# Kernel optimization log

Measured on AMD Instinct MI355X. Metric: run time of the kernel, lower is better.

## Reference

```python
import jax, jax.numpy as jnp
import numpy as np
import math

H = 8  # num_heads
SCALE = 1.0 / math.sqrt(512.0)  # original divides by sqrt(dim_V), not sqrt(head_dim)


def setup_inputs() -> dict:
    key = jax.random.key(0)
    ks = jax.random.split(key, 16)
    B, N, D = 32, 512, 512
    s = 1.0 / math.sqrt(D)
    return {
        "Q": jax.random.normal(ks[0], (B, N, D), jnp.float32),
        "K": jax.random.normal(ks[1], (B, N, D), jnp.float32),
        "Wq": jax.random.normal(ks[2], (D, D), jnp.float32) * s,
        "bq": jnp.zeros((D,), jnp.float32),
        "Wk": jax.random.normal(ks[3], (D, D), jnp.float32) * s,
        "bk": jnp.zeros((D,), jnp.float32),
        "Wv": jax.random.normal(ks[4], (D, D), jnp.float32) * s,
        "bv": jnp.zeros((D,), jnp.float32),
        "Wo": jax.random.normal(ks[5], (D, D), jnp.float32) * s,
        "bo": jnp.zeros((D,), jnp.float32),
        "W1": jax.random.normal(ks[6], (D, D), jnp.float32) * s,
        "b1": jnp.zeros((D,), jnp.float32),
        "W2": jax.random.normal(ks[7], (D, D), jnp.float32) * s,
        "b2": jnp.zeros((D,), jnp.float32),
    }


def reference(Q, K, Wq, bq, Wk, bk, Wv, bv, Wo, bo, W1, b1, W2, b2):
    B, Nq, D = Q.shape
    dh = D // H
    # projections (torch Linear: x @ W.T + b)
    q = (Q @ Wq.T + bq).reshape(B, Nq, H, dh)
    k = (K @ Wk.T + bk).reshape(B, K.shape[1], H, dh)
    v = (K @ Wv.T + bv).reshape(B, K.shape[1], H, dh)
    # scores: [B, H, Nq, Nk], scaled by 1/sqrt(dim_V)
    scores = jnp.einsum("bqhd,bkhd->bhqk", q, k) * SCALE
    # NOTE: original softmax is over dim=1 of [H*B, Nq, Nk] == the QUERY axis
    A = jax.nn.softmax(scores, axis=2)
    attn = jnp.einsum("bhqk,bkhd->bqhd", A, v).reshape(B, Nq, D)
    out = Q + (attn @ Wo.T + bo)  # dropout p=0.0
    ffn = jax.nn.relu(out @ W1.T + b1) @ W2.T + b2
    return out + ffn
```

## Files before the change

### kernel.cpp

```cpp
#include <hip/hip_runtime.h>
#include <stdint.h>

#define SCALE_ 0.044194173824159216f
#define QSC_ (0.044194173824159216f * 1.4426950408889634f)

typedef __attribute__((ext_vector_type(8))) short bf16x8;
typedef __attribute__((ext_vector_type(4))) float f32x4;
typedef __attribute__((ext_vector_type(16))) float f32x16;
typedef __attribute__((ext_vector_type(2))) unsigned int uint2v;

__device__ __forceinline__ ushort f2b(float f) {
  union { float f; uint32_t u; } v; v.f = f;
  return (ushort)((v.u + 0x7fffu + ((v.u >> 16) & 1u)) >> 16);
}
__device__ __forceinline__ uint32_t cvtpk(float lo, float hi) {
  uint32_t r; asm("v_cvt_pk_bf16_f32 %0, %1, %2" : "=v"(r) : "v"(lo), "v"(hi)); return r;
}
__device__ __forceinline__ float ex2(float x) {
  float r; asm("v_exp_f32 %0, %1" : "=v"(r) : "v"(x)); return r;
}
__device__ __forceinline__ void gld16(void* lds, const void* g) {
  __builtin_amdgcn_global_load_lds(
      (const __attribute__((address_space(1))) uint32_t*)g,
      (__attribute__((address_space(3))) uint32_t*)lds, 16, 0, 0);
}

__global__ __launch_bounds__(256)
void k_cvt(const float* __restrict__ Q, const float* __restrict__ K,
           const float* __restrict__ w0, const float* __restrict__ w1,
           const float* __restrict__ w2, const float* __restrict__ w3,
           const float* __restrict__ w4, const float* __restrict__ w5,
           ushort* __restrict__ Qb, ushort* __restrict__ Kb, ushort* __restrict__ Wb)
{
  const long long NQ = 8388608LL, NW = 262144LL;
  long long i = ((long long)blockIdx.x * 256 + threadIdx.x) * 4;
  const float* src; ushort* dst; long long off;
  if (i < NQ)        { src = Q; dst = Qb; off = i; }
  else if (i < 2*NQ) { src = K; dst = Kb; off = i - NQ; }
  else {
    long long j = i - 2*NQ; int seg = (int)(j / NW); off = j - (long long)seg * NW;
    switch (seg) { case 0: src = w0; break; case 1: src = w1; break; case 2: src = w2; break;
                   case 3: src = w3; break; case 4: src = w4; break; default: src = w5; }
    dst = Wb + (size_t)seg * NW;
  }
  float4 v = *(const float4*)(src + off);
  ushort4 o = make_ushort4(f2b(v.x), f2b(v.y), f2b(v.z), f2b(v.w));
  *(ushort4*)(dst + off) = o;
}

template<int EPI>
__device__ __forceinline__ void gemm_body(const ushort* __restrict__ A, const ushort* __restrict__ Bw,
                                          const float* __restrict__ bias, const float* __restrict__ extra,
                                          float* __restrict__ outf, ushort* __restrict__ outb,
                                          char* lds, int m0, int n0, float os)
{
  const int t = threadIdx.x;
  const int w = t >> 6, lane = t & 63;
  const int wm = w >> 1, wn = w & 1;
  const int rA = lane & 15, g = lane >> 4;

  const ushort* srcA[4]; int ldsA[4];
#pragma unroll
  for (int j = 0; j < 4; j++) {
    int L = (t + j*512) * 16;
    int U = L ^ (((L >> 7) & 7) << 4);
    srcA[j] = A + (size_t)(m0 + (U >> 7))*512 + ((U & 127) >> 1);
    ldsA[j] = L;
  }
  const ushort* srcB[2]; int ldsB[2];
#pragma unroll
  for (int j = 0; j < 2; j++) {
    int L = (t + j*512) * 16;
    int U = L ^ (((L >> 7) & 7) << 4);
    srcB[j] = Bw + (size_t)(n0 + (U >> 7))*512 + ((U & 127) >> 1);
    ldsB[j] = 32768 + L;
  }

#define STAGE_A(ti) do { char* bb_ = lds + ((ti) % 3) * 49152; \
    _Pragma("unroll") \
    for (int j = 0; j < 4; j++) gld16(bb_ + ldsA[j], srcA[j] + (ti)*64); } while (0)
#define STAGE_B(ti) do { char* bb_ = lds + ((ti) % 3) * 49152; \
    _Pragma("unroll") \
    for (int j = 0; j < 2; j++) gld16(bb_ + ldsB[j], srcB[j] + (ti)*64); } while (0)

  STAGE_A(0); STAGE_B(0);
  STAGE_A(1); STAGE_B(1);

  f32x4 acc[4][4] = {};
  for (int i = 0; i < 8; i++) {
    if (i < 7) asm volatile("s_waitcnt vmcnt(6)" ::: "memory");
    else       asm volatile("s_waitcnt vmcnt(0)" ::: "memory");
    __builtin_amdgcn_s_barrier();
    __builtin_amdgcn_sched_barrier(0);
    const char* bufc = lds + (i % 3) * 49152;

    bf16x8 afA[4], bfA[4];
#pragma unroll
    for (int m = 0; m < 4; m++) {
      int row = wm*64 + m*16 + rA;
      afA[m] = *(const bf16x8*)(bufc + ((row*128 + g*16) ^ ((row & 7) << 4)));
    }
#pragma unroll
    for (int n = 0; n < 4; n++) {
      int row = wn*64 + n*16 + rA;
      bfA[n] = *(const bf16x8*)(bufc + 32768 + ((row*128 + g*16) ^ ((row & 7) << 4)));
    }
    if (i < 6) STAGE_A(i + 2);
    __builtin_amdgcn_s_barrier();
    __builtin_amdgcn_sched_barrier(0);

    bf16x8 afB[4], bfB[4];
#pragma unroll
    for (int m = 0; m < 4; m++) {
      int row = wm*64 + m*16 + rA;
      afB[m] = *(const bf16x8*)(bufc + ((row*128 + 64 + g*16) ^ ((row & 7) << 4)));
    }
#pragma unroll
    for (int n = 0; n < 4; n++) {
      int row = wn*64 + n*16 + rA;
      bfB[n] = *(const bf16x8*)(bufc + 32768 + ((row*128 + 64 + g*16) ^ ((row & 7) << 4)));
    }
    if (i < 6) STAGE_B(i + 2);
    __builtin_amdgcn_s_setprio(1);
#pragma unroll
    for (int m = 0; m < 4; m++)
#pragma unroll
      for (int n = 0; n < 4; n++)
        acc[m][n] = __builtin_amdgcn_mfma_f32_16x16x32_bf16(afA[m], bfA[n], acc[m][n], 0, 0, 0);
    __builtin_amdgcn_s_setprio(0);
    __builtin_amdgcn_s_barrier();
    __builtin_amdgcn_sched_barrier(0);

    __builtin_amdgcn_s_setprio(1);
#pragma unroll
    for (int m = 0; m < 4; m++)
#pragma unroll
      for (int n = 0; n < 4; n++)
        acc[m][n] = __builtin_amdgcn_mfma_f32_16x16x32_bf16(afB[m], bfB[n], acc[m][n], 0, 0, 0);
    __builtin_amdgcn_s_setprio(0);
  }
#undef STAGE_A
#undef STAGE_B

#pragma unroll
  for (int m = 0; m < 4; m++)
#pragma unroll
    for (int n = 0; n < 4; n++) {
      int col = n0 + wn*64 + n*16 + rA;
      float bb = bias[col];
      if (EPI == 4) {
        int b = m0 >> 9, k0 = m0 & 511;
        int hh = col >> 6, dl = col & 63;
        int kg = k0 + wm*64 + m*16 + g*4;
        float v0 = acc[m][n][0] + bb, v1 = acc[m][n][1] + bb;
        float v2 = acc[m][n][2] + bb, v3 = acc[m][n][3] + bb;
        uint2 pk;
        pk.x = (uint32_t)f2b(v0) | ((uint32_t)f2b(v1) << 16);
        pk.y = (uint32_t)f2b(v2) | ((uint32_t)f2b(v3) << 16);
        *(uint2*)(outb + ((size_t)((b*8 + hh)*64 + dl)*512 + kg)) = pk;
      } else {
#pragma unroll
        for (int r = 0; r < 4; r++) {
          int row = m0 + wm*64 + m*16 + g*4 + r;
          size_t idx = (size_t)row*512 + col;
          float v = acc[m][n][r] + bb;
          if (EPI == 0)      outb[idx] = f2b(v * os);
          else if (EPI == 1) { float o = extra[idx] + v; outf[idx] = o; outb[idx] = f2b(o); }
          else if (EPI == 2) outb[idx] = f2b(v > 0.f ? v : 0.f);
          else               outf[idx] += v;
        }
      }
    }
}

template<int EPI>
__global__ __launch_bounds__(512, 2)
void k_gemm(const ushort* __restrict__ A, const ushort* __restrict__ Bw,
            const float* __restrict__ bias, const float* __restrict__ extra,
            float* __restrict__ outf, ushort* __restrict__ outb)
{
  __shared__ __align__(16) char lds[3*49152];
  gemm_body<EPI>(A, Bw, bias, extra, outf, outb, lds, blockIdx.x*256, blockIdx.y*128, 1.0f);
}

__global__ __launch_bounds__(512, 2)
void k_gemm_qkv(const ushort* __restrict__ Qb, const ushort* __restrict__ Kb,
                const ushort* __restrict__ Wb, const float* __restrict__ bq,
                const float* __restrict__ bk, const float* __restrict__ bvv,
                ushort* __restrict__ qkout, ushort* __restrict__ vpT)
{
  __shared__ __align__(16) char lds[3*49152];
  int z = blockIdx.z;
  if (z == 2) {
    gemm_body<4>(Kb, Wb + 2*(size_t)262144, bvv, nullptr, nullptr,
                 vpT, lds, blockIdx.x*256, blockIdx.y*128, 1.0f);
  } else {
    const ushort* A = (z == 0) ? Qb : Kb;
    const float* bias = (z == 0) ? bq : bk;
    float os = (z == 0) ? QSC_ : 1.0f;
    gemm_body<0>(A, Wb + (size_t)z*262144, bias, nullptr, nullptr,
                 qkout + (size_t)z*8388608, lds, blockIdx.x*256, blockIdx.y*128, os);
  }
}

__global__ __launch_bounds__(512, 2)
void k_att2(const ushort* __restrict__ qp, const ushort* __restrict__ kp,
            const ushort* __restrict__ vpT, float* __restrict__ zinv,
            ushort* __restrict__ attn)
{
  __shared__ __align__(16) char kt[65536];
  __shared__ __align__(16) char vt[65536];
  __shared__ __align__(16) char qpr[32768];
  int bh = blockIdx.x;
  int b = bh >> 3, h = bh & 7;
  int t = threadIdx.x, w = t >> 6, lane = t & 63;
  int rA = lane & 15, g = lane >> 4;
  const ushort* kbase = kp + (size_t)(b*512)*512 + h*64;
  const ushort* qbase = qp + (size_t)(b*512)*512 + h*64;
  const ushort* vbase = vpT + (size_t)bh*64*512;

#pragma unroll
  for (int i = 0; i < 8; i++) {
    int c = i*512 + t; int row = c >> 3, sl = c & 7;
    gld16(kt + c*16, kbase + (size_t)row*512 + ((sl ^ (row & 7))*8));
  }
#define STAGE_Q(buf, qb) do { \
    _Pragma("unroll") \
    for (int i = 0; i < 2; i++) { \
      int c = i*512 + t; int row = c >> 3, sl = c & 7; \
      gld16(qpr + (buf)*16384 + c*16, \
            qbase + (size_t)((qb)*128 + row)*512 + ((sl ^ (row & 7))*8)); } } while (0)
  STAGE_Q(0, 0);
  STAGE_Q(1, 1);
#pragma unroll
  for (int i = 0; i < 8; i++) {
    int c = i*512 + t; int d = c >> 6, sl = c & 63;
    gld16(vt + c*16, vbase + (size_t)d*512 + ((sl ^ (d & 7))*8));
  }

  asm volatile("s_waitcnt vmcnt(10)" ::: "memory");
  __builtin_amdgcn_s_barrier();
  __builtin_amdgcn_sched_barrier(0);
  bf16x8 kf[4][2];
#pragma unroll
  for (int n = 0; n < 4; n++)
#pragma unroll
    for (int ks = 0; ks < 2; ks++) {
      int k = w*64 + n*16 + rA;
      kf[n][ks] = *(const bf16x8*)(kt + k*128 + (((ks*4 + g) ^ (k & 7))*16));
    }
  float Zacc[4] = {0.f, 0.f, 0.f, 0.f};
  for (int qb = 0; qb < 4; qb++) {
    if (qb == 1)      { asm volatile("s_waitcnt vmcnt(10)" ::: "memory"); }
    else if (qb == 2) { asm volatile("s_waitcnt vmcnt(2)" ::: "memory"); }
    else if (qb == 3) { asm volatile("s_waitcnt vmcnt(0)" ::: "memory"); }
    if (qb) { __builtin_amdgcn_s_barrier(); __builtin_amdgcn_sched_barrier(0); }
    const char* qtb = qpr + (qb & 1)*16384;
    f32x4 acc[8][4] = {};
#pragma unroll
    for (int ks = 0; ks < 2; ks++) {
      bf16x8 af[8];
#pragma unroll
      for (int m = 0; m < 8; m++) {
        int q = m*16 + rA;
        af[m] = *(const bf16x8*)(qtb + q*128 + (((ks*4 + g) ^ (q & 7))*16));
      }
      __builtin_amdgcn_s_setprio(1);
#pragma unroll
      for (int m = 0; m < 8; m++)
#pragma unroll
        for (int n = 0; n < 4; n++)
          acc[m][n] = __builtin_amdgcn_mfma_f32_16x16x32_bf16(af[m], kf[n][ks], acc[m][n], 0, 0, 0);
      __builtin_amdgcn_s_setprio(0);
    }
    if (qb < 3) __builtin_amdgcn_s_barrier();
    if (qb < 2) STAGE_Q(qb & 1, qb + 2);
#pragma unroll
    for (int m = 0; m < 8; m++)
#pragma unroll
      for (int n = 0; n < 4; n++) {
        float s = 0.f;
#pragma unroll
        for (int r = 0; r < 4; r++) s += ex2(acc[m][n][r]);
        Zacc[n] += s;
      }
  }
#undef STAGE_Q
#pragma unroll
  for (int n = 0; n < 4; n++) {
    float v = Zacc[n];
    v += __shfl_xor(v, 16);
    v += __shfl_xor(v, 32);
    if (lane < 16) ((float*)qpr)[w*64 + n*16 + lane] = 1.0f / v;
  }
  __syncthreads();

  const int l31 = lane & 31, hi5 = lane >> 5;
  bf16x8 qf2[2][4];
#pragma unroll
  for (int qb = 0; qb < 2; qb++)
#pragma unroll
    for (int ksd = 0; ksd < 4; ksd++)
      qf2[qb][ksd] = *(const bf16x8*)(qbase + (size_t)(w*64 + qb*32 + l31)*512 + ksd*16 + hi5*8);
  const float* zl = (const float*)qpr;
  f32x16 oacc[2][2] = {};
  for (int kc = 0; kc < 16; kc++) {
    bf16x8 kf2[4];
#pragma unroll
    for (int ksd = 0; ksd < 4; ksd++) {
      int k = kc*32 + l31;
      kf2[ksd] = *(const bf16x8*)(kt + k*128 + (((ksd*2 + hi5) ^ (k & 7))*16));
    }
    bf16x8 vf2[2][2];
#pragma unroll
    for (int db = 0; db < 2; db++)
#pragma unroll
      for (int ks = 0; ks < 2; ks++) {
        int d = db*32 + l31;
        vf2[db][ks] = *(const bf16x8*)(vt + d*1024 + (((kc*4 + ks*2 + hi5) ^ (d & 7))*16));
      }
    f32x4 zv[4];
#pragma unroll
    for (int j = 0; j < 4; j++)
      zv[j] = *(const f32x4*)(zl + kc*32 + j*8 + hi5*4);
#pragma unroll
    for (int qb = 0; qb < 2; qb++) {
      f32x16 s = {};
      __builtin_amdgcn_s_setprio(1);
#pragma unroll
      for (int ksd = 0; ksd < 4; ksd++)
        s = __builtin_amdgcn_mfma_f32_32x32x16_bf16(kf2[ksd], qf2[qb][ksd], s, 0, 0, 0);
      __builtin_amdgcn_s_setprio(0);
      float e[16];
#pragma unroll
      for (int r = 0; r < 16; r++) e[r] = ex2(s[r]) * zv[r >> 2][r & 3];
      uint32_t x0 = cvtpk(e[0], e[1]),   y0 = cvtpk(e[4], e[5]);
      uint32_t x1 = cvtpk(e[2], e[3]),   y1 = cvtpk(e[6], e[7]);
      uint32_t x2 = cvtpk(e[8], e[9]),   y2 = cvtpk(e[12], e[13]);
      uint32_t x3 = cvtpk(e[10], e[11]), y3 = cvtpk(e[14], e[15]);
      uint2v r0 = __builtin_amdgcn_permlane32_swap(x0, y0, false, false);
      uint2v r1 = __builtin_amdgcn_permlane32_swap(x1, y1, false, false);
      uint2v r2 = __builtin_amdgcn_permlane32_swap(x2, y2, false, false);
      uint2v r3 = __builtin_amdgcn_permlane32_swap(x3, y3, false, false);
      union { uint32_t u[4]; bf16x8 v; } p0, p1;
      p0.u[0] = r0[0]; p0.u[1] = r1[0]; p0.u[2] = r0[1]; p0.u[3] = r1[1];
      p1.u[0] = r2[0]; p1.u[1] = r3[0]; p1.u[2] = r2[1]; p1.u[3] = r3[1];
      __builtin_amdgcn_s_setprio(1);
#pragma unroll
      for (int db = 0; db < 2; db++) {
        oacc[qb][db] = __builtin_amdgcn_mfma_f32_32x32x16_bf16(p0.v, vf2[db][0], oacc[qb][db], 0, 0, 0);
        oacc[qb][db] = __builtin_amdgcn_mfma_f32_32x32x16_bf16(p1.v, vf2[db][1], oacc[qb][db], 0, 0, 0);
      }
      __builtin_amdgcn_s_setprio(0);
    }
  }
#pragma unroll
  for (int qb = 0; qb < 2; qb++)
#pragma unroll
    for (int db = 0; db < 2; db++)
#pragma unroll
      for (int r = 0; r < 16; r++) {
        int q = w*64 + qb*32 + (r & 3) + 8*(r >> 2) + 4*hi5;
        int d = db*32 + l31;
        attn[(size_t)(b*512 + q)*512 + h*64 + d] = f2b(oacc[qb][db][r]);
      }
}

extern "C" void kernel_launch(void* const* d_in, const int* in_sizes, int n_in,
                              void* d_out, int out_size, void* d_ws, size_t ws_size,
                              hipStream_t stream) {
  const float* Q  = (const float*)d_in[0];
  const float* K  = (const float*)d_in[1];
  const float* Wq = (const float*)d_in[2];
  const float* bq = (const float*)d_in[3];
  const float* Wk = (const float*)d_in[4];
  const float* bk = (const float*)d_in[5];
  const float* Wv = (const float*)d_in[6];
  const float* bv = (const float*)d_in[7];
  const float* Wo = (const float*)d_in[8];
  const float* bo = (const float*)d_in[9];
  const float* W1 = (const float*)d_in[10];
  const float* b1 = (const float*)d_in[11];
  const float* W2 = (const float*)d_in[12];
  const float* b2 = (const float*)d_in[13];
  float* out = (float*)d_out;

  const size_t SZ = (size_t)16384 * 512;
  ushort* Qb   = (ushort*)d_ws;
  ushort* Kb   = Qb + SZ;
  ushort* qp   = Kb + SZ;
  ushort* kp   = qp + SZ;
  ushort* vpT  = kp + SZ;
  ushort* Wb   = vpT + SZ;
  float*  zinv = (float*)(Wb + 6 * (size_t)262144);
  ushort* attn = Qb;
  ushort* outb = Kb;
  ushort* h1   = vpT;

  k_cvt<<<dim3(17920), dim3(256), 0, stream>>>(Q, K, Wq, Wk, Wv, Wo, W1, W2, Qb, Kb, Wb);
  k_gemm_qkv<<<dim3(64, 4, 3), dim3(512), 0, stream>>>(Qb, Kb, Wb, bq, bk, bv, qp, vpT);
  k_att2<<<dim3(256), dim3(512), 0, stream>>>(qp, kp, vpT, zinv, attn);
  k_gemm<1><<<dim3(64, 4), dim3(512), 0, stream>>>(attn, Wb + 3*(size_t)262144, bo, Q, out, outb);
  k_gemm<2><<<dim3(64, 4), dim3(512), 0, stream>>>(outb, Wb + 4*(size_t)262144, b1, nullptr, nullptr, h1);
  k_gemm<3><<<dim3(64, 4), dim3(512), 0, stream>>>(h1, Wb + 5*(size_t)262144, b2, nullptr, out, nullptr);
}
```

Before: 148.3 us.

## Fuse fp32-to-bf16 conversion of Q/K into QKV projection GEMM loads

The separate conversion pass over Q and K is removed. The QKV GEMM now loads fp32 activations into registers, packs them to bf16 with v_cvt_pk_bf16_f32, and writes them to swizzled LDS, software-pipelined two tiles ahead. Weights keep a small dedicated conversion kernel. The generic GEMM main loop is also restructured to load both K-halves of fragments and issue all staging before one barrier, cutting barriers per iteration. The cost is extra register pressure and VALU/LDS-store work inside the QKV GEMM, and K is re-read as fp32 by two GEMM z-slices.

```diff
diff --git a/kernel.cpp b/kernel.cpp
--- a/kernel.cpp
+++ b/kernel.cpp
@@ -26,33 +26,28 @@
 }
 
 __global__ __launch_bounds__(256)
-void k_cvt(const float* __restrict__ Q, const float* __restrict__ K,
-           const float* __restrict__ w0, const float* __restrict__ w1,
-           const float* __restrict__ w2, const float* __restrict__ w3,
-           const float* __restrict__ w4, const float* __restrict__ w5,
-           ushort* __restrict__ Qb, ushort* __restrict__ Kb, ushort* __restrict__ Wb)
+void k_cvtw(const float* __restrict__ w0, const float* __restrict__ w1,
+            const float* __restrict__ w2, const float* __restrict__ w3,
+            const float* __restrict__ w4, const float* __restrict__ w5,
+            ushort* __restrict__ Wb)
 {
-  const long long NQ = 8388608LL, NW = 262144LL;
-  long long i = ((long long)blockIdx.x * 256 + threadIdx.x) * 4;
-  const float* src; ushort* dst; long long off;
-  if (i < NQ)        { src = Q; dst = Qb; off = i; }
-  else if (i < 2*NQ) { src = K; dst = Kb; off = i - NQ; }
-  else {
-    long long j = i - 2*NQ; int seg = (int)(j / NW); off = j - (long long)seg * NW;
-    switch (seg) { case 0: src = w0; break; case 1: src = w1; break; case 2: src = w2; break;
-                   case 3: src = w3; break; case 4: src = w4; break; default: src = w5; }
-    dst = Wb + (size_t)seg * NW;
-  }
+  const int NW = 262144;
+  int i = (blockIdx.x * 256 + threadIdx.x) * 4;
+  int seg = i >> 18;
+  int off = i & (NW - 1);
+  const float* src;
+  switch (seg) { case 0: src = w0; break; case 1: src = w1; break; case 2: src = w2; break;
+                 case 3: src = w3; break; case 4: src = w4; break; default: src = w5; }
   float4 v = *(const float4*)(src + off);
   ushort4 o = make_ushort4(f2b(v.x), f2b(v.y), f2b(v.z), f2b(v.w));
-  *(ushort4*)(dst + off) = o;
+  *(ushort4*)(Wb + (size_t)seg * NW + off) = o;
 }
 
 template<int EPI>
 __device__ __forceinline__ void gemm_body(const ushort* __restrict__ A, const ushort* __restrict__ Bw,
                                           const float* __restrict__ bias, const float* __restrict__ extra,
                                           float* __restrict__ outf, ushort* __restrict__ outb,
-                                          char* lds, int m0, int n0, float os)
+                                          char* lds, int m0, int n0)
 {
   const int t = threadIdx.x;
   const int w = t >> 6, lane = t & 63;
@@ -94,44 +89,27 @@
     __builtin_amdgcn_sched_barrier(0);
     const char* bufc = lds + (i % 3) * 49152;
 
-    bf16x8 afA[4], bfA[4];
+    bf16x8 afA[4], bfA[4], afB[4], bfB[4];
 #pragma unroll
     for (int m = 0; m < 4; m++) {
       int row = wm*64 + m*16 + rA;
       afA[m] = *(const bf16x8*)(bufc + ((row*128 + g*16) ^ ((row & 7) << 4)));
+      afB[m] = *(const bf16x8*)(bufc + ((row*128 + 64 + g*16) ^ ((row & 7) << 4)));
     }
 #pragma unroll
     for (int n = 0; n < 4; n++) {
       int row = wn*64 + n*16 + rA;
       bfA[n] = *(const bf16x8*)(bufc + 32768 + ((row*128 + g*16) ^ ((row & 7) << 4)));
-    }
-    if (i < 6) STAGE_A(i + 2);
-    __builtin_amdgcn_s_barrier();
+      bfB[n] = *(const bf16x8*)(bufc + 32768 + ((row*128 + 64 + g*16) ^ ((row & 7) << 4)));
+    }
+    if (i < 6) { STAGE_A(i + 2); STAGE_B(i + 2); }
     __builtin_amdgcn_sched_barrier(0);
-
-    bf16x8 afB[4], bfB[4];
-#pragma unroll
-    for (int m = 0; m < 4; m++) {
-      int row = wm*64 + m*16 + rA;
-      afB[m] = *(const bf16x8*)(bufc + ((row*128 + 64 + g*16) ^ ((row & 7) << 4)));
-    }
-#pragma unroll
-    for (int n = 0; n < 4; n++) {
-      int row = wn*64 + n*16 + rA;
-      bfB[n] = *(const bf16x8*)(bufc + 32768 + ((row*128 + 64 + g*16) ^ ((row & 7) << 4)));
-    }
-    if (i < 6) STAGE_B(i + 2);
     __builtin_amdgcn_s_setprio(1);
 #pragma unroll
     for (int m = 0; m < 4; m++)
 #pragma unroll
       for (int n = 0; n < 4; n++)
         acc[m][n] = __builtin_amdgcn_mfma_f32_16x16x32_bf16(afA[m], bfA[n], acc[m][n], 0, 0, 0);
-    __builtin_amdgcn_s_setprio(0);
-    __builtin_amdgcn_s_barrier();
-    __builtin_amdgcn_sched_barrier(0);
-
-    __builtin_amdgcn_s_setprio(1);
 #pragma unroll
     for (int m = 0; m < 4; m++)
 #pragma unroll
@@ -141,6 +119,144 @@
   }
 #undef STAGE_A
 #undef STAGE_B
+
+#pragma unroll
+  for (int m = 0; m < 4; m++)
+#pragma unroll
+    for (int n = 0; n < 4; n++) {
+      int col = n0 + wn*64 + n*16 + rA;
+      float bb = bias[col];
+#pragma unroll
+      for (int r = 0; r < 4; r++) {
+        int row = m0 + wm*64 + m*16 + g*4 + r;
+        size_t idx = (size_t)row*512 + col;
+        float v = acc[m][n][r] + bb;
+        if (EPI == 1)      { float o = extra[idx] + v; outf[idx] = o; outb[idx] = f2b(o); }
+        else if (EPI == 2) outb[idx] = f2b(v > 0.f ? v : 0.f);
+        else               outf[idx] += v;
+      }
+    }
+}
+
+template<int EPI>
+__global__ __launch_bounds__(512, 2)
+void k_gemm(const ushort* __restrict__ A, const ushort* __restrict__ Bw,
+            const float* __restrict__ bias, const float* __restrict__ extra,
+            float* __restrict__ outf, ushort* __restrict__ outb)
+{
+  __shared__ __align__(16) char lds[3*49152];
+  gemm_body<EPI>(A, Bw, bias, extra, outf, outb, lds, blockIdx.x*256, blockIdx.y*128);
+}
+
+template<int EPI>
+__device__ __forceinline__ void gemm_f32a_body(const float* __restrict__ A32, const ushort* __restrict__ Bw,
+                                               const float* __restrict__ bias,
+                                               float* __restrict__ outf, ushort* __restrict__ outb,
+                                               char* lds, int m0, int n0, float os)
+{
+  const int t = threadIdx.x;
+  const int w = t >> 6, lane = t & 63;
+  const int wm = w >> 1, wn = w & 1;
+  const int rA = lane & 15, g = lane >> 4;
+
+  const float* srcA[4]; int ldsA[4];
+#pragma unroll
+  for (int j = 0; j < 4; j++) {
+    int L = (t + j*512) * 16;
+    int U = L ^ (((L >> 7) & 7) << 4);
+    srcA[j] = A32 + (size_t)(m0 + (U >> 7))*512 + ((U & 127) >> 1);
+    ldsA[j] = L;
+  }
+  const ushort* srcB[2]; int ldsB[2];
+#pragma unroll
+  for (int j = 0; j < 2; j++) {
+    int L = (t + j*512) * 16;
+    int U = L ^ (((L >> 7) & 7) << 4);
+    srcB[j] = Bw + (size_t)(n0 + (U >> 7))*512 + ((U & 127) >> 1);
+    ldsB[j] = 32768 + L;
+  }
+
+#define QLA(ti, R) do { \
+    _Pragma("unroll") \
+    for (int j = 0; j < 4; j++) { \
+      R[2*j]   = *(const float4*)(srcA[j] + (ti)*64); \
+      R[2*j+1] = *(const float4*)(srcA[j] + (ti)*64 + 4); } } while (0)
+#define QWA(ti, R) do { char* bb_ = lds + ((ti) % 3) * 49152; \
+    _Pragma("unroll") \
+    for (int j = 0; j < 4; j++) { \
+      uint4 qq; \
+      qq.x = cvtpk(R[2*j].x,   R[2*j].y); \
+      qq.y = cvtpk(R[2*j].z,   R[2*j].w); \
+      qq.z = cvtpk(R[2*j+1].x, R[2*j+1].y); \
+      qq.w = cvtpk(R[2*j+1].z, R[2*j+1].w); \
+      *(uint4*)(bb_ + ldsA[j]) = qq; } } while (0)
+#define QSB(ti) do { char* bb_ = lds + ((ti) % 3) * 49152; \
+    _Pragma("unroll") \
+    for (int j = 0; j < 2; j++) gld16(bb_ + ldsB[j], srcB[j] + (ti)*64); } while (0)
+
+  float4 a0[8], a1[8];
+  QLA(0, a0);
+  __builtin_amdgcn_sched_barrier(0);
+  QLA(1, a1);
+  __builtin_amdgcn_sched_barrier(0);
+  QSB(0); QSB(1);
+  __builtin_amdgcn_sched_barrier(0);
+  asm volatile("s_waitcnt vmcnt(12)" ::: "memory");
+  QWA(0, a0);
+
+  f32x4 acc[4][4] = {};
+
+#define QITER(i, RI, RW) do { \
+    if ((i) == 0)      asm volatile("s_waitcnt vmcnt(2) lgkmcnt(0)" ::: "memory"); \
+    else if ((i) == 7) asm volatile("s_waitcnt vmcnt(0) lgkmcnt(0)" ::: "memory"); \
+    else               asm volatile("s_waitcnt vmcnt(10) lgkmcnt(0)" ::: "memory"); \
+    __builtin_amdgcn_s_barrier(); \
+    __builtin_amdgcn_sched_barrier(0); \
+    const char* bufc = lds + ((i) % 3) * 49152; \
+    bf16x8 afA[4], bfA[4], afB[4], bfB[4]; \
+    _Pragma("unroll") \
+    for (int m = 0; m < 4; m++) { \
+      int row = wm*64 + m*16 + rA; \
+      afA[m] = *(const bf16x8*)(bufc + ((row*128 + g*16) ^ ((row & 7) << 4))); \
+      afB[m] = *(const bf16x8*)(bufc + ((row*128 + 64 + g*16) ^ ((row & 7) << 4))); \
+    } \
+    _Pragma("unroll") \
+    for (int n = 0; n < 4; n++) { \
+      int row = wn*64 + n*16 + rA; \
+      bfA[n] = *(const bf16x8*)(bufc + 32768 + ((row*128 + g*16) ^ ((row & 7) << 4))); \
+      bfB[n] = *(const bf16x8*)(bufc + 32768 + ((row*128 + 64 + g*16) ^ ((row & 7) << 4))); \
+    } \
+    if ((i) < 6) QLA((i) + 2, RI); \
+    __builtin_amdgcn_sched_barrier(0); \
+    if ((i) < 7) QWA((i) + 1, RW); \
+    if ((i) < 6) QSB((i) + 2); \
+    __builtin_amdgcn_sched_barrier(0); \
+    __builtin_amdgcn_s_setprio(1); \
+    _Pragma("unroll") \
+    for (int m = 0; m < 4; m++) \
+      _Pragma("unroll") \
+      for (int n = 0; n < 4; n++) \
+        acc[m][n] = __builtin_amdgcn_mfma_f32_16x16x32_bf16(afA[m], bfA[n], acc[m][n], 0, 0, 0); \
+    _Pragma("unroll") \
+    for (int m = 0; m < 4; m++) \
+      _Pragma("unroll") \
+      for (int n = 0; n < 4; n++) \
+        acc[m][n] = __builtin_amdgcn_mfma_f32_16x16x32_bf16(afB[m], bfB[n], acc[m][n], 0, 0, 0); \
+    __builtin_amdgcn_s_setprio(0); \
+  } while (0)
+
+  QITER(0, a0, a1);
+  QITER(1, a1, a0);
+  QITER(2, a0, a1);
+  QITER(3, a1, a0);
+  QITER(4, a0, a1);
+  QITER(5, a1, a0);
+  QITER(6, a0, a1);
+  QITER(7, a1, a0);
+#undef QITER
+#undef QLA
+#undef QWA
+#undef QSB
 
 #pragma unroll
   for (int m = 0; m < 4; m++)
@@ -163,43 +279,29 @@
         for (int r = 0; r < 4; r++) {
           int row = m0 + wm*64 + m*16 + g*4 + r;
           size_t idx = (size_t)row*512 + col;
-          float v = acc[m][n][r] + bb;
-          if (EPI == 0)      outb[idx] = f2b(v * os);
-          else if (EPI == 1) { float o = extra[idx] + v; outf[idx] = o; outb[idx] = f2b(o); }
-          else if (EPI == 2) outb[idx] = f2b(v > 0.f ? v : 0.f);
-          else               outf[idx] += v;
+          outb[idx] = f2b((acc[m][n][r] + bb) * os);
         }
       }
     }
 }
 
-template<int EPI>
 __global__ __launch_bounds__(512, 2)
-void k_gemm(const ushort* __restrict__ A, const ushort* __restrict__ Bw,
-            const float* __restrict__ bias, const float* __restrict__ extra,
-            float* __restrict__ outf, ushort* __restrict__ outb)
-{
-  __shared__ __align__(16) char lds[3*49152];
-  gemm_body<EPI>(A, Bw, bias, extra, outf, outb, lds, blockIdx.x*256, blockIdx.y*128, 1.0f);
-}
-
-__global__ __launch_bounds__(512, 2)
-void k_gemm_qkv(const ushort* __restrict__ Qb, const ushort* __restrict__ Kb,
-                const ushort* __restrict__ Wb, const float* __restrict__ bq,
-                const float* __restrict__ bk, const float* __restrict__ bvv,
-                ushort* __restrict__ qkout, ushort* __restrict__ vpT)
+void k_gemm_qkvf(const float* __restrict__ Qf, const float* __restrict__ Kf,
+                 const ushort* __restrict__ Wb, const float* __restrict__ bq,
+                 const float* __restrict__ bk, const float* __restrict__ bvv,
+                 ushort* __restrict__ qkout, ushort* __restrict__ vpT)
 {
   __shared__ __align__(16) char lds[3*49152];
   int z = blockIdx.z;
   if (z == 2) {
-    gemm_body<4>(Kb, Wb + 2*(size_t)262144, bvv, nullptr, nullptr,
-                 vpT, lds, blockIdx.x*256, blockIdx.y*128, 1.0f);
+    gemm_f32a_body<4>(Kf, Wb + 2*(size_t)262144, bvv, nullptr, vpT,
+                      lds, blockIdx.x*256, blockIdx.y*128, 1.0f);
+  } else if (z == 1) {
+    gemm_f32a_body<0>(Kf, Wb + (size_t)262144, bk, nullptr, qkout + (size_t)8388608,
+                      lds, blockIdx.x*256, blockIdx.y*128, 1.0f);
   } else {
-    const ushort* A = (z == 0) ? Qb : Kb;
-    const float* bias = (z == 0) ? bq : bk;
-    float os = (z == 0) ? QSC_ : 1.0f;
-    gemm_body<0>(A, Wb + (size_t)z*262144, bias, nullptr, nullptr,
-                 qkout + (size_t)z*8388608, lds, blockIdx.x*256, blockIdx.y*128, os);
+    gemm_f32a_body<0>(Qf, Wb, bq, nullptr, qkout,
+                      lds, blockIdx.x*256, blockIdx.y*128, QSC_);
   }
 }
 
@@ -386,19 +488,17 @@
   float* out = (float*)d_out;
 
   const size_t SZ = (size_t)16384 * 512;
-  ushort* Qb   = (ushort*)d_ws;
-  ushort* Kb   = Qb + SZ;
-  ushort* qp   = Kb + SZ;
+  ushort* attn = (ushort*)d_ws;
+  ushort* outb = attn + SZ;
+  ushort* qp   = outb + SZ;
   ushort* kp   = qp + SZ;
   ushort* vpT  = kp + SZ;
   ushort* Wb   = vpT + SZ;
   float*  zinv = (float*)(Wb + 6 * (size_t)262144);
-  ushort* attn = Qb;
-  ushort* outb = Kb;
   ushort* h1   = vpT;
 
-  k_cvt<<<dim3(17920), dim3(256), 0, stream>>>(Q, K, Wq, Wk, Wv, Wo, W1, W2, Qb, Kb, Wb);
-  k_gemm_qkv<<<dim3(64, 4, 3), dim3(512), 0, stream>>>(Qb, Kb, Wb, bq, bk, bv, qp, vpT);
+  k_cvtw<<<dim3(1536), dim3(256), 0, stream>>>(Wq, Wk, Wv, Wo, W1, W2, Wb);
+  k_gemm_qkvf<<<dim3(64, 4, 3), dim3(512), 0, stream>>>(Q, K, Wb, bq, bk, bv, qp, vpT);
   k_att2<<<dim3(256), dim3(512), 0, stream>>>(qp, kp, vpT, zinv, attn);
   k_gemm<1><<<dim3(64, 4), dim3(512), 0, stream>>>(attn, Wb + 3*(size_t)262144, bo, Q, out, outb);
   k_gemm<2><<<dim3(64, 4), dim3(512), 0, stream>>>(outb, Wb + 4*(size_t)262144, b1, nullptr, nullptr, h1);
```

Result: no change. 146.5 us (-1.2%).

## Fuse fp32-to-bf16 conversion of Q/K into projection GEMMs and share K tiles for K/V

Applied to the files above, without the earlier changes.

The separate pass that converted the full Q and K activations to bf16 is removed. The projection GEMMs now stream fp32 A tiles into LDS and convert them to bf16 in registers before the MFMAs. The K and V projections are fused into one kernel that reuses each loaded K tile against both weight matrices. The shared GEMM loop is also simplified to one barrier and one staging step per k-step. This is meant to remove a large read-and-write round trip through memory, at the cost of double the A-tile LDS traffic, lower occupancy (launch bounds of 1) and extra register pressure from the dual accumulators.

```diff
diff --git a/kernel.cpp b/kernel.cpp
--- a/kernel.cpp
+++ b/kernel.cpp
@@ -26,33 +26,28 @@
 }
 
 __global__ __launch_bounds__(256)
-void k_cvt(const float* __restrict__ Q, const float* __restrict__ K,
-           const float* __restrict__ w0, const float* __restrict__ w1,
-           const float* __restrict__ w2, const float* __restrict__ w3,
-           const float* __restrict__ w4, const float* __restrict__ w5,
-           ushort* __restrict__ Qb, ushort* __restrict__ Kb, ushort* __restrict__ Wb)
-{
-  const long long NQ = 8388608LL, NW = 262144LL;
-  long long i = ((long long)blockIdx.x * 256 + threadIdx.x) * 4;
-  const float* src; ushort* dst; long long off;
-  if (i < NQ)        { src = Q; dst = Qb; off = i; }
-  else if (i < 2*NQ) { src = K; dst = Kb; off = i - NQ; }
-  else {
-    long long j = i - 2*NQ; int seg = (int)(j / NW); off = j - (long long)seg * NW;
-    switch (seg) { case 0: src = w0; break; case 1: src = w1; break; case 2: src = w2; break;
-                   case 3: src = w3; break; case 4: src = w4; break; default: src = w5; }
-    dst = Wb + (size_t)seg * NW;
-  }
+void k_cvtw(const float* __restrict__ w0, const float* __restrict__ w1,
+            const float* __restrict__ w2, const float* __restrict__ w3,
+            const float* __restrict__ w4, const float* __restrict__ w5,
+            ushort* __restrict__ Wb)
+{
+  const int NW = 262144;
+  int i = (blockIdx.x * 256 + threadIdx.x) * 4;
+  int seg = i >> 18;
+  int off = i & (NW - 1);
+  const float* src;
+  switch (seg) { case 0: src = w0; break; case 1: src = w1; break; case 2: src = w2; break;
+                 case 3: src = w3; break; case 4: src = w4; break; default: src = w5; }
   float4 v = *(const float4*)(src + off);
   ushort4 o = make_ushort4(f2b(v.x), f2b(v.y), f2b(v.z), f2b(v.w));
-  *(ushort4*)(dst + off) = o;
+  *(ushort4*)(Wb + (size_t)seg * NW + off) = o;
 }
 
 template<int EPI>
 __device__ __forceinline__ void gemm_body(const ushort* __restrict__ A, const ushort* __restrict__ Bw,
                                           const float* __restrict__ bias, const float* __restrict__ extra,
                                           float* __restrict__ outf, ushort* __restrict__ outb,
-                                          char* lds, int m0, int n0, float os)
+                                          char* lds, int m0, int n0)
 {
   const int t = threadIdx.x;
   const int w = t >> 6, lane = t & 63;
@@ -76,15 +71,13 @@
     ldsB[j] = 32768 + L;
   }
 
-#define STAGE_A(ti) do { char* bb_ = lds + ((ti) % 3) * 49152; \
+#define STAGE_T(ti) do { char* bb_ = lds + ((ti) % 3) * 49152; \
     _Pragma("unroll") \
-    for (int j = 0; j < 4; j++) gld16(bb_ + ldsA[j], srcA[j] + (ti)*64); } while (0)
-#define STAGE_B(ti) do { char* bb_ = lds + ((ti) % 3) * 49152; \
+    for (int j = 0; j < 4; j++) gld16(bb_ + ldsA[j], srcA[j] + (ti)*64); \
     _Pragma("unroll") \
     for (int j = 0; j < 2; j++) gld16(bb_ + ldsB[j], srcB[j] + (ti)*64); } while (0)
 
-  STAGE_A(0); STAGE_B(0);
-  STAGE_A(1); STAGE_B(1);
+  STAGE_T(0); STAGE_T(1);
 
   f32x4 acc[4][4] = {};
   for (int i = 0; i < 8; i++) {
@@ -94,44 +87,27 @@
     __builtin_amdgcn_sched_barrier(0);
     const char* bufc = lds + (i % 3) * 49152;
 
-    bf16x8 afA[4], bfA[4];
+    bf16x8 afA[4], bfA[4], afB[4], bfB[4];
 #pragma unroll
     for (int m = 0; m < 4; m++) {
       int row = wm*64 + m*16 + rA;
       afA[m] = *(const bf16x8*)(bufc + ((row*128 + g*16) ^ ((row & 7) << 4)));
+      afB[m] = *(const bf16x8*)(bufc + ((row*128 + 64 + g*16) ^ ((row & 7) << 4)));
     }
 #pragma unroll
     for (int n = 0; n < 4; n++) {
       int row = wn*64 + n*16 + rA;
       bfA[n] = *(const bf16x8*)(bufc + 32768 + ((row*128 + g*16) ^ ((row & 7) << 4)));
-    }
-    if (i < 6) STAGE_A(i + 2);
-    __builtin_amdgcn_s_barrier();
+      bfB[n] = *(const bf16x8*)(bufc + 32768 + ((row*128 + 64 + g*16) ^ ((row & 7) << 4)));
+    }
+    if (i < 6) STAGE_T(i + 2);
     __builtin_amdgcn_sched_barrier(0);
-
-    bf16x8 afB[4], bfB[4];
-#pragma unroll
-    for (int m = 0; m < 4; m++) {
-      int row = wm*64 + m*16 + rA;
-      afB[m] = *(const bf16x8*)(bufc + ((row*128 + 64 + g*16) ^ ((row & 7) << 4)));
-    }
-#pragma unroll
-    for (int n = 0; n < 4; n++) {
-      int row = wn*64 + n*16 + rA;
-      bfB[n] = *(const bf16x8*)(bufc + 32768 + ((row*128 + 64 + g*16) ^ ((row & 7) << 4)));
-    }
-    if (i < 6) STAGE_B(i + 2);
     __builtin_amdgcn_s_setprio(1);
 #pragma unroll
     for (int m = 0; m < 4; m++)
 #pragma unroll
       for (int n = 0; n < 4; n++)
         acc[m][n] = __builtin_amdgcn_mfma_f32_16x16x32_bf16(afA[m], bfA[n], acc[m][n], 0, 0, 0);
-    __builtin_amdgcn_s_setprio(0);
-    __builtin_amdgcn_s_barrier();
-    __builtin_amdgcn_sched_barrier(0);
-
-    __builtin_amdgcn_s_setprio(1);
 #pragma unroll
     for (int m = 0; m < 4; m++)
 #pragma unroll
@@ -139,8 +115,7 @@
         acc[m][n] = __builtin_amdgcn_mfma_f32_16x16x32_bf16(afB[m], bfB[n], acc[m][n], 0, 0, 0);
     __builtin_amdgcn_s_setprio(0);
   }
-#undef STAGE_A
-#undef STAGE_B
+#undef STAGE_T
 
 #pragma unroll
   for (int m = 0; m < 4; m++)
@@ -148,27 +123,14 @@
     for (int n = 0; n < 4; n++) {
       int col = n0 + wn*64 + n*16 + rA;
       float bb = bias[col];
-      if (EPI == 4) {
-        int b = m0 >> 9, k0 = m0 & 511;
-        int hh = col >> 6, dl = col & 63;
-        int kg = k0 + wm*64 + m*16 + g*4;
-        float v0 = acc[m][n][0] + bb, v1 = acc[m][n][1] + bb;
-        float v2 = acc[m][n][2] + bb, v3 = acc[m][n][3] + bb;
-        uint2 pk;
-        pk.x = (uint32_t)f2b(v0) | ((uint32_t)f2b(v1) << 16);
-        pk.y = (uint32_t)f2b(v2) | ((uint32_t)f2b(v3) << 16);
-        *(uint2*)(outb + ((size_t)((b*8 + hh)*64 + dl)*512 + kg)) = pk;
-      } else {
-#pragma unroll
-        for (int r = 0; r < 4; r++) {
-          int row = m0 + wm*64 + m*16 + g*4 + r;
-          size_t idx = (size_t)row*512 + col;
-          float v = acc[m][n][r] + bb;
-          if (EPI == 0)      outb[idx] = f2b(v * os);
-          else if (EPI == 1) { float o = extra[idx] + v; outf[idx] = o; outb[idx] = f2b(o); }
-          else if (EPI == 2) outb[idx] = f2b(v > 0.f ? v : 0.f);
-          else               outf[idx] += v;
-        }
+#pragma unroll
+      for (int r = 0; r < 4; r++) {
+        int row = m0 + wm*64 + m*16 + g*4 + r;
+        size_t idx = (size_t)row*512 + col;
+        float v = acc[m][n][r] + bb;
+        if (EPI == 1)      { float o = extra[idx] + v; outf[idx] = o; outb[idx] = f2b(o); }
+        else if (EPI == 2) outb[idx] = f2b(v > 0.f ? v : 0.f);
+        else               outf[idx] += v;
       }
     }
 }
@@ -180,27 +142,149 @@
             float* __restrict__ outf, ushort* __restrict__ outb)
 {
   __shared__ __align__(16) char lds[3*49152];
-  gemm_body<EPI>(A, Bw, bias, extra, outf, outb, lds, blockIdx.x*256, blockIdx.y*128, 1.0f);
-}
-
-__global__ __launch_bounds__(512, 2)
-void k_gemm_qkv(const ushort* __restrict__ Qb, const ushort* __restrict__ Kb,
-                const ushort* __restrict__ Wb, const float* __restrict__ bq,
-                const float* __restrict__ bk, const float* __restrict__ bvv,
-                ushort* __restrict__ qkout, ushort* __restrict__ vpT)
+  gemm_body<EPI>(A, Bw, bias, extra, outf, outb, lds, blockIdx.x*256, blockIdx.y*128);
+}
+
+template<int DUAL>
+__device__ __forceinline__ void proj_body(const float* __restrict__ A32, const ushort* __restrict__ B0w,
+                                          const ushort* __restrict__ B1w,
+                                          const float* __restrict__ bias0, const float* __restrict__ bias1,
+                                          ushort* __restrict__ out0, ushort* __restrict__ vpT,
+                                          char* lds, int m0, int n0, float os)
+{
+  const int t = threadIdx.x;
+  const int w = t >> 6, lane = t & 63;
+  const int wm = w >> 1, wn = w & 1;
+  const int rA = lane & 15, g = lane >> 4;
+  const int BUF = DUAL ? 49152 : 40960;
+  const int L = DUAL ? 6 : 5;
+
+  const float* srcA[4]; int ldsA[4];
+#pragma unroll
+  for (int j = 0; j < 4; j++) {
+    int Lb = (t + j*512) * 16;
+    int U = Lb ^ (((Lb >> 7) & 7) << 4);
+    srcA[j] = A32 + (size_t)(m0 + (U >> 7))*512 + ((U & 127) >> 2);
+    ldsA[j] = Lb;
+  }
+  const ushort* srcB0; const ushort* srcB1; int ldsB;
+  {
+    int Lb = t * 16;
+    int U = Lb ^ (((Lb >> 6) & 3) << 4);
+    int row = U >> 6, col = (U & 63) >> 1;
+    srcB0 = B0w + (size_t)(n0 + row)*512 + col;
+    srcB1 = DUAL ? (B1w + (size_t)(n0 + row)*512 + col) : srcB0;
+    ldsB = 32768 + Lb;
+  }
+
+#define PSTAGE(ti) do { char* bb_ = lds + ((ti) % 3) * BUF; \
+    _Pragma("unroll") \
+    for (int j = 0; j < 4; j++) gld16(bb_ + ldsA[j], srcA[j] + (ti)*32); \
+    gld16(bb_ + ldsB, srcB0 + (ti)*32); \
+    if (DUAL) gld16(bb_ + 8192 + ldsB, srcB1 + (ti)*32); } while (0)
+
+  PSTAGE(0); PSTAGE(1);
+
+  f32x4 acc0[4][4] = {};
+  f32x4 acc1[4][4] = {};
+  for (int i = 0; i < 16; i++) {
+    if (i < 15) { if (DUAL) asm volatile("s_waitcnt vmcnt(6)" ::: "memory");
+                  else      asm volatile("s_waitcnt vmcnt(5)" ::: "memory"); }
+    else          asm volatile("s_waitcnt vmcnt(0)" ::: "memory");
+    __builtin_amdgcn_s_barrier();
+    __builtin_amdgcn_sched_barrier(0);
+    const char* bufc = lds + (i % 3) * BUF;
+
+    bf16x8 af[4];
+#pragma unroll
+    for (int m = 0; m < 4; m++) {
+      int row = wm*64 + m*16 + rA;
+      int o0 = (row*128 + g*32) ^ ((row & 7) << 4);
+      f32x4 lo = *(const f32x4*)(bufc + o0);
+      f32x4 hi = *(const f32x4*)(bufc + (o0 ^ 16));
+      union { uint32_t u[4]; bf16x8 v; } af_;
+      af_.u[0] = cvtpk(lo[0], lo[1]); af_.u[1] = cvtpk(lo[2], lo[3]);
+      af_.u[2] = cvtpk(hi[0], hi[1]); af_.u[3] = cvtpk(hi[2], hi[3]);
+      af[m] = af_.v;
+    }
+    bf16x8 bf0[4];
+#pragma unroll
+    for (int n = 0; n < 4; n++) {
+      int row = wn*64 + n*16 + rA;
+      bf0[n] = *(const bf16x8*)(bufc + 32768 + ((row*64 + g*16) ^ ((row & 3) << 4)));
+    }
+    if (i < 14) PSTAGE(i + 2);
+    __builtin_amdgcn_sched_barrier(0);
+    __builtin_amdgcn_s_setprio(1);
+#pragma unroll
+    for (int m = 0; m < 4; m++)
+#pragma unroll
+      for (int n = 0; n < 4; n++)
+        acc0[m][n] = __builtin_amdgcn_mfma_f32_16x16x32_bf16(af[m], bf0[n], acc0[m][n], 0, 0, 0);
+    __builtin_amdgcn_s_setprio(0);
+    if (DUAL) {
+      bf16x8 bf1[4];
+#pragma unroll
+      for (int n = 0; n < 4; n++) {
+        int row = wn*64 + n*16 + rA;
+        bf1[n] = *(const bf16x8*)(bufc + 40960 + ((row*64 + g*16) ^ ((row & 3) << 4)));
+      }
+      __builtin_amdgcn_s_setprio(1);
+#pragma unroll
+      for (int m = 0; m < 4; m++)
+#pragma unroll
+        for (int n = 0; n < 4; n++)
+          acc1[m][n] = __builtin_amdgcn_mfma_f32_16x16x32_bf16(af[m], bf1[n], acc1[m][n], 0, 0, 0);
+      __builtin_amdgcn_s_setprio(0);
+    }
+  }
+#undef PSTAGE
+
+#pragma unroll
+  for (int m = 0; m < 4; m++)
+#pragma unroll
+    for (int n = 0; n < 4; n++) {
+      int col = n0 + wn*64 + n*16 + rA;
+      {
+        float bb = bias0[col];
+#pragma unroll
+        for (int r = 0; r < 4; r++) {
+          int row = m0 + wm*64 + m*16 + g*4 + r;
+          out0[(size_t)row*512 + col] = f2b((acc0[m][n][r] + bb) * os);
+        }
+      }
+      if (DUAL) {
+        float bb = bias1[col];
+        int b = m0 >> 9, k0 = m0 & 511;
+        int hh = col >> 6, dl = col & 63;
+        int kg = k0 + wm*64 + m*16 + g*4;
+        float v0 = acc1[m][n][0] + bb, v1 = acc1[m][n][1] + bb;
+        float v2 = acc1[m][n][2] + bb, v3 = acc1[m][n][3] + bb;
+        uint2 pk;
+        pk.x = (uint32_t)f2b(v0) | ((uint32_t)f2b(v1) << 16);
+        pk.y = (uint32_t)f2b(v2) | ((uint32_t)f2b(v3) << 16);
+        *(uint2*)(vpT + ((size_t)((b*8 + hh)*64 + dl)*512 + kg)) = pk;
+      }
+    }
+}
+
+__global__ __launch_bounds__(512, 1)
+void k_projq(const float* __restrict__ Qf, const ushort* __restrict__ Wb,
+             const float* __restrict__ bq, ushort* __restrict__ qp)
+{
+  __shared__ __align__(16) char lds[3*40960];
+  proj_body<0>(Qf, Wb, nullptr, bq, nullptr, qp, nullptr,
+               lds, blockIdx.x*256, blockIdx.y*128, QSC_);
+}
+
+__global__ __launch_bounds__(512, 1)
+void k_projkv(const float* __restrict__ Kf, const ushort* __restrict__ Wb,
+              const float* __restrict__ bk, const float* __restrict__ bvv,
+              ushort* __restrict__ kp, ushort* __restrict__ vpT)
 {
   __shared__ __align__(16) char lds[3*49152];
-  int z = blockIdx.z;
-  if (z == 2) {
-    gemm_body<4>(Kb, Wb + 2*(size_t)262144, bvv, nullptr, nullptr,
-                 vpT, lds, blockIdx.x*256, blockIdx.y*128, 1.0f);
-  } else {
-    const ushort* A = (z == 0) ? Qb : Kb;
-    const float* bias = (z == 0) ? bq : bk;
-    float os = (z == 0) ? QSC_ : 1.0f;
-    gemm_body<0>(A, Wb + (size_t)z*262144, bias, nullptr, nullptr,
-                 qkout + (size_t)z*8388608, lds, blockIdx.x*256, blockIdx.y*128, os);
-  }
+  proj_body<1>(Kf, Wb + (size_t)262144, Wb + 2*(size_t)262144, bk, bvv, kp, vpT,
+               lds, blockIdx.x*256, blockIdx.y*128, 1.0f);
 }
 
 __global__ __launch_bounds__(512, 2)
@@ -386,19 +470,18 @@
   float* out = (float*)d_out;
 
   const size_t SZ = (size_t)16384 * 512;
-  ushort* Qb   = (ushort*)d_ws;
-  ushort* Kb   = Qb + SZ;
-  ushort* qp   = Kb + SZ;
+  ushort* attn = (ushort*)d_ws;
+  ushort* outb = attn + SZ;
+  ushort* qp   = outb + SZ;
   ushort* kp   = qp + SZ;
   ushort* vpT  = kp + SZ;
   ushort* Wb   = vpT + SZ;
   float*  zinv = (float*)(Wb + 6 * (size_t)262144);
-  ushort* attn = Qb;
-  ushort* outb = Kb;
   ushort* h1   = vpT;
 
-  k_cvt<<<dim3(17920), dim3(256), 0, stream>>>(Q, K, Wq, Wk, Wv, Wo, W1, W2, Qb, Kb, Wb);
-  k_gemm_qkv<<<dim3(64, 4, 3), dim3(512), 0, stream>>>(Qb, Kb, Wb, bq, bk, bv, qp, vpT);
+  k_cvtw<<<dim3(1536), dim3(256), 0, stream>>>(Wq, Wk, Wv, Wo, W1, W2, Wb);
+  k_projq<<<dim3(64, 4), dim3(512), 0, stream>>>(Q, Wb, bq, qp);
+  k_projkv<<<dim3(64, 4), dim3(512), 0, stream>>>(K, Wb, bk, bv, kp, vpT);
   k_att2<<<dim3(256), dim3(512), 0, stream>>>(qp, kp, vpT, zinv, attn);
   k_gemm<1><<<dim3(64, 4), dim3(512), 0, stream>>>(attn, Wb + 3*(size_t)262144, bo, Q, out, outb);
   k_gemm<2><<<dim3(64, 4), dim3(512), 0, stream>>>(outb, Wb + 4*(size_t)262144, b1, nullptr, nullptr, h1);
```

New measurement: 141.7 us. 4.5% less time.
